# Kernel tuning notes

Hardware: AMD Instinct MI355X
Metric: run time of the kernel (lower is better)

Reference implementation:

```python
import jax, jax.numpy as jnp
import numpy as np

N = 50000   # nodes per graph stream
E = 800000  # edges per graph stream
G = 100     # graphs in batch
FIN, H = 74, 256


def setup_inputs() -> dict:
    key = jax.random.key(0)
    ks = jax.random.split(key, 16)
    d = {
        'xl': jax.random.normal(ks[0], (N, FIN), jnp.float32),
        'xr': jax.random.normal(ks[1], (N, FIN), jnp.float32),
        'src_l': jax.random.randint(ks[2], (E,), 0, N, jnp.int32),
        'dst_l': jax.random.randint(ks[3], (E,), 0, N, jnp.int32),
        'src_r': jax.random.randint(ks[4], (E,), 0, N, jnp.int32),
        'dst_r': jax.random.randint(ks[5], (E,), 0, N, jnp.int32),
        'gid_l': jnp.sort(jax.random.randint(ks[6], (N,), 0, G, jnp.int32)),
        'gid_r': jnp.sort(jax.random.randint(ks[7], (N,), 0, G, jnp.int32)),
        'W0': jax.random.normal(ks[8], (FIN, H), jnp.float32) / np.sqrt(FIN),
        'b0': jnp.zeros((H,), jnp.float32),
        'W1': jax.random.normal(ks[9], (H, H), jnp.float32) / np.sqrt(H),
        'b1': jnp.zeros((H,), jnp.float32),
        'W2': jax.random.normal(ks[10], (H, H), jnp.float32) / np.sqrt(H),
        'b2': jnp.zeros((H,), jnp.float32),
        'Wf1': jax.random.normal(ks[11], (2 * H, H), jnp.float32) / np.sqrt(2 * H),
        'bf1': jnp.zeros((H,), jnp.float32),
        'Wf2': jax.random.normal(ks[12], (H, 1), jnp.float32) / np.sqrt(H),
        'bf2': jnp.zeros((1,), jnp.float32),
    }
    return d


def _deg_isqrt(idx, n):
    deg = jax.ops.segment_sum(jnp.ones_like(idx, jnp.float32), idx, num_segments=n)
    return jax.lax.rsqrt(jnp.maximum(deg, 1.0))


def _graph_conv(x, src, dst, do_isq, di_isq, W, b):
    # DGL GraphConv, norm='both': h = relu(D_in^{-1/2} A D_out^{-1/2} X W + b)
    h = (x * do_isq[:, None]) @ W            # transform-first (in_feats >= out for layer0 path is fine mathematically)
    agg = jax.ops.segment_sum(h[src], dst, num_segments=x.shape[0])
    return jax.nn.relu(agg * di_isq[:, None] + b)


def reference(xl, xr, src_l, dst_l, src_r, dst_r, gid_l, gid_r,
              W0, b0, W1, b1, W2, b2, Wf1, bf1, Wf2, bf2):
    do_l, di_l = _deg_isqrt(src_l, N), _deg_isqrt(dst_l, N)
    do_r, di_r = _deg_isqrt(src_r, N), _deg_isqrt(dst_r, N)
    Ws, bs = (W0, W1, W2), (b0, b1, b2)
    hl, hr = xl, xr
    for W, b in zip(Ws, bs):  # shared weights across both graph streams
        hl = _graph_conv(hl, src_l, dst_l, do_l, di_l, W, b)
        hr = _graph_conv(hr, src_r, dst_r, do_r, di_r, W, b)
    pl = jax.ops.segment_sum(hl, gid_l, num_segments=G)  # dgl.sum_nodes
    pr = jax.ops.segment_sum(hr, gid_r, num_segments=G)
    z = jnp.concatenate([pl, pr], axis=-1)               # [G, 2H]
    return jax.nn.relu(z @ Wf1 + bf1) @ Wf2 + bf2        # [G, 1]
```

## Files before the change

kernel.cpp:

```cpp
#include <hip/hip_runtime.h>

#define N_NODES 50000
#define N_EDGES 800000
#define N_GRAPHS 100
#define FIN_DIM 74
#define K0 96
#define H_DIM 256
#define EG 3125
#define XS_BLKS 18750
#define WCONV_BLKS 608
#define AGG0_BLKS 3128
#define AGGH_BLKS 6256
#define GEMM_BLKS 782
#define POOL_BLKS 782
#define SCAN_BLOCKS 196

typedef float f32x4 __attribute__((ext_vector_type(4)));
typedef unsigned int u32x4 __attribute__((ext_vector_type(4)));
typedef unsigned short us8 __attribute__((ext_vector_type(8)));
typedef __bf16 bf16x8 __attribute__((ext_vector_type(8)));

__device__ __forceinline__ unsigned short f2bf(float x) {
    unsigned u = __builtin_bit_cast(unsigned, x);
    u += 0x7fff + ((u >> 16) & 1);
    return (unsigned short)(u >> 16);
}
__device__ __forceinline__ float bf2f(unsigned short h) {
    return __builtin_bit_cast(float, (unsigned)h << 16);
}
__device__ __forceinline__ void acc8(float* a, us8 v) {
    u32x4 w = __builtin_bit_cast(u32x4, v);
    #pragma unroll
    for (int i = 0; i < 4; ++i) {
        a[2 * i]     += __builtin_bit_cast(float, w[i] << 16);
        a[2 * i + 1] += __builtin_bit_cast(float, w[i] & 0xffff0000u);
    }
}


__device__ __forceinline__ void hist_body(int bid, const int* __restrict__ src,
                                          const int* __restrict__ dst,
                                          int* __restrict__ cs, int* __restrict__ fc,
                                          int* __restrict__ rk) {
    int e = bid * 256 + threadIdx.x;
    if (e < N_EDGES) {
        rk[e] = atomicAdd(&fc[dst[e]], 1);
        atomicAdd(&cs[src[e]], 1);
    }
}

__device__ __forceinline__ void scat_body(int bid, const int* __restrict__ src,
                                          const int* __restrict__ dst,
                                          const int* __restrict__ rp,
                                          const int* __restrict__ rk,
                                          int* __restrict__ col) {
    int e = bid * 256 + threadIdx.x;
    if (e < N_EDGES) {
        int d = dst[e];
        col[rp[d] + rk[e]] = src[e];
    }
}

__device__ __forceinline__ void xscale_body(int bid, const float* __restrict__ x,
                                            const float* __restrict__ dso,
                                            unsigned short* __restrict__ xp) {
    int id = bid * 256 + threadIdx.x;
    int n = id / 96, f = id - n * 96;
    float v = (f < FIN_DIM) ? x[(size_t)n * FIN_DIM + f] * dso[n] : 0.f;
    xp[(size_t)(f >> 4) * (N_NODES * 16) + (size_t)n * 16 + (f & 15)] = f2bf(v);
}

__device__ __forceinline__ void wconv_body(int bid, const float* __restrict__ W0,
                                           const float* __restrict__ W1,
                                           const float* __restrict__ W2,
                                           unsigned short* __restrict__ Wt) {
    int id = bid * 256 + threadIdx.x;
    if (id < 256 * 96) {
        int n = id / 96, k = id - n * 96;
        float v = (k < FIN_DIM) ? W0[(size_t)k * H_DIM + n] : 0.f;
        Wt[id] = f2bf(v);
    } else if (id < 256 * 96 + 65536) {
        int id2 = id - 256 * 96;
        int n = id2 >> 8, k = id2 & 255;
        Wt[id] = f2bf(W1[(size_t)k * H_DIM + n]);
    } else {
        int id3 = id - 256 * 96 - 65536;
        int n = id3 >> 8, k = id3 & 255;
        Wt[id] = f2bf(W2[(size_t)k * H_DIM + n]);
    }
}

template<int SW, int NACT, int NSL>
__device__ __forceinline__ void agg_body(int abid, int cg,
                                         const unsigned short* __restrict__ h,
                                         const int* __restrict__ rp,
                                         const int* __restrict__ col,
                                         unsigned short* __restrict__ A) {
    const int CPB = SW / 8;
    const int NPB = 256 / CPB;
    if (cg >= NSL) return;
    int slot = threadIdx.x & (CPB - 1);
    int n = (abid >> 3) * NPB + threadIdx.x / CPB;
    if (n >= N_NODES) return;
    unsigned short* dst = A + (size_t)cg * (N_NODES * SW) + (size_t)n * SW + slot * 8;
    if (cg >= NACT) { us8 z = {}; *(us8*)dst = z; return; }
    const unsigned short* hs = h + (size_t)cg * (N_NODES * SW) + slot * 8;
    int beg = rp[n], end = rp[n + 1];
    float a[8] = {};
    int j = beg;
    for (; j + 3 < end; j += 4) {
        int s0 = col[j], s1 = col[j + 1], s2 = col[j + 2], s3 = col[j + 3];
        us8 v0 = *(const us8*)(hs + (size_t)s0 * SW);
        us8 v1 = *(const us8*)(hs + (size_t)s1 * SW);
        us8 v2 = *(const us8*)(hs + (size_t)s2 * SW);
        us8 v3 = *(const us8*)(hs + (size_t)s3 * SW);
        acc8(a, v0); acc8(a, v1); acc8(a, v2); acc8(a, v3);
    }
    for (; j < end; ++j)
        acc8(a, *(const us8*)(hs + (size_t)col[j] * SW));
    us8 r;
    #pragma unroll
    for (int i = 0; i < 8; ++i) r[i] = f2bf(a[i]);
    *(us8*)dst = r;
}

__device__ __forceinline__ void pool_body(int nb, const unsigned short* __restrict__ h,
                                          const int* __restrict__ gid,
                                          float* __restrict__ pool) {
    int n0 = nb * 64;
    int f = threadIdx.x;
    const unsigned short* hf = h + (size_t)(f >> 5) * (N_NODES * 32) + (f & 31);
    int end = min(n0 + 64, N_NODES);
    float acc = 0.0f;
    int gcur = gid[n0];
    for (int i = n0; i < end; ++i) {
        int g = gid[i];
        if (g != gcur) {
            atomicAdd(&pool[(size_t)gcur * H_DIM + f], acc);
            acc = 0.0f;
            gcur = g;
        }
        acc += bf2f(hf[(size_t)i * 32]);
    }
    atomicAdd(&pool[(size_t)gcur * H_DIM + f], acc);
}

template<int K, int SW>
__device__ __forceinline__ void gemm_body(int id, const unsigned short* __restrict__ A,
                                          const unsigned short* __restrict__ Wt,
                                          const float* __restrict__ bias,
                                          const float* __restrict__ dsi,
                                          const float* __restrict__ scale,
                                          unsigned short* __restrict__ C,
                                          unsigned short* smem) {
    unsigned short (*Ah)[40] = (unsigned short(*)[40])smem;
    unsigned short (*Bh)[40] = (unsigned short(*)[40])(smem + 128 * 40);
    const int M = N_NODES;

    int tid = threadIdx.x;
    int lane = tid & 63, wid = tid >> 6;
    int wm = (wid >> 1) * 64, wn = (wid & 1) * 64;
    int bm = (id >> 1) * 128, bn = (id & 1) * 128;

    f32x4 acc[4][4] = {};
    int r0 = wm + (lane & 15);
    int c0 = wn + (lane & 15);
    int kA = (lane >> 4) * 8;

    for (int k0 = 0; k0 < K; k0 += 32) {
        #pragma unroll
        for (int i = 0; i < 2; ++i) {
            int q = tid + i * 256;
            int row = q >> 2, k8 = (q & 3) * 8;
            int gm = bm + row;
            int kk = k0 + k8;
            us8 v = {};
            if (gm < M)
                v = *(const us8*)(A + (size_t)(kk / SW) * ((size_t)N_NODES * SW)
                                    + (size_t)gm * SW + (kk % SW));
            *(us8*)&Ah[row][k8] = v;
        }
        {
            int colx = tid & 127, kg = tid >> 7;
            const unsigned short* wsrc = Wt + (size_t)(bn + colx) * K + k0 + kg * 16;
            us8 w0 = *(const us8*)(wsrc);
            us8 w1 = *(const us8*)(wsrc + 8);
            *(us8*)&Bh[colx][kg * 16] = w0;
            *(us8*)&Bh[colx][kg * 16 + 8] = w1;
        }
        __syncthreads();

        bf16x8 ah[4], bh[4];
        #pragma unroll
        for (int m = 0; m < 4; ++m)
            ah[m] = __builtin_bit_cast(bf16x8, *(const us8*)&Ah[r0 + m * 16][kA]);
        #pragma unroll
        for (int n = 0; n < 4; ++n)
            bh[n] = __builtin_bit_cast(bf16x8, *(const us8*)&Bh[c0 + n * 16][kA]);

        #pragma unroll
        for (int m = 0; m < 4; ++m)
            #pragma unroll
            for (int n = 0; n < 4; ++n)
                acc[m][n] = __builtin_amdgcn_mfma_f32_16x16x32_bf16(ah[m], bh[n], acc[m][n], 0, 0, 0);
        __syncthreads();
    }

    int rowq = (lane >> 4) * 4;
    #pragma unroll
    for (int n = 0; n < 4; ++n) {
        int gn = bn + wn + n * 16 + (lane & 15);
        float bv = bias[gn];
        unsigned short* cs = C + (size_t)(gn >> 5) * (N_NODES * 32) + (gn & 31);
        #pragma unroll
        for (int m = 0; m < 4; ++m) {
            #pragma unroll
            for (int j = 0; j < 4; ++j) {
                int gm = bm + wm + m * 16 + rowq + j;
                if (gm < M) {
                    float r = fmaxf(acc[m][n][j] * dsi[gm] + bv, 0.0f);
                    if (scale) r *= scale[gm];
                    cs[(size_t)gm * 32] = f2bf(r);
                }
            }
        }
    }
}


__device__ __forceinline__ int block_excl_scan(int v, int* wsums) {
    int lane = threadIdx.x & 63, w = threadIdx.x >> 6;
    int x = v;
    #pragma unroll
    for (int ofs = 1; ofs < 64; ofs <<= 1) {
        int y = __shfl_up(x, ofs, 64);
        if (lane >= ofs) x += y;
    }
    if (lane == 63) wsums[w] = x;
    __syncthreads();
    int wo = 0;
    #pragma unroll
    for (int k = 0; k < 4; ++k) if (k < w) wo += wsums[k];
    return wo + x - v;
}

__global__ void k_hist2(const float* __restrict__ W0, const float* __restrict__ W1,
                        const float* __restrict__ W2, unsigned short* __restrict__ Wt,
                        const int* __restrict__ srcL, const int* __restrict__ dstL,
                        int* __restrict__ csL, int* __restrict__ fcL, int* __restrict__ rkL,
                        const int* __restrict__ srcR, const int* __restrict__ dstR,
                        int* __restrict__ csR, int* __restrict__ fcR, int* __restrict__ rkR) {
    int bid = blockIdx.x;
    if (bid < WCONV_BLKS)           wconv_body(bid, W0, W1, W2, Wt);
    else if (bid < WCONV_BLKS + EG) hist_body(bid - WCONV_BLKS, srcL, dstL, csL, fcL, rkL);
    else                            hist_body(bid - WCONV_BLKS - EG, srcR, dstR, csR, fcR, rkR);
}

__global__ void deg_scan1_kernel(const int* __restrict__ csL, const int* __restrict__ fcL,
                                 float* __restrict__ dsoL, float* __restrict__ dsiL,
                                 int* __restrict__ rpL, int* __restrict__ bsL,
                                 const int* __restrict__ csR, const int* __restrict__ fcR,
                                 float* __restrict__ dsoR, float* __restrict__ dsiR,
                                 int* __restrict__ rpR, int* __restrict__ bsR) {
    const int* cs = blockIdx.y ? csR : csL;
    const int* fc = blockIdx.y ? fcR : fcL;
    float* dso = blockIdx.y ? dsoR : dsoL;
    float* dsi = blockIdx.y ? dsiR : dsiL;
    int* rp = blockIdx.y ? rpR : rpL;
    int* bs = blockIdx.y ? bsR : bsL;
    __shared__ int ws[4];
    int i = blockIdx.x * 256 + threadIdx.x;
    int v = 0;
    if (i < N_NODES) {
        dso[i] = rsqrtf(fmaxf((float)cs[i], 1.0f));
        v = fc[i];
        dsi[i] = rsqrtf(fmaxf((float)v, 1.0f));
    }
    int ex = block_excl_scan(v, ws);
    if (i < N_NODES) rp[i] = ex;
    if (threadIdx.x == 255) bs[blockIdx.x] = ex + v;
}

__global__ void scan2_kernel(int* __restrict__ bsL, int* __restrict__ bsR, int nb) {
    int* bs = blockIdx.y ? bsR : bsL;
    __shared__ int ws[4];
    int i = threadIdx.x;
    int v = (i < nb) ? bs[i] : 0;
    int ex = block_excl_scan(v, ws);
    __syncthreads();
    if (i < nb) bs[i] = ex;
}

__global__ void scan3_kernel(int* __restrict__ rpL, const int* __restrict__ bsL,
                             int* __restrict__ rpR, const int* __restrict__ bsR) {
    int* rp = blockIdx.y ? rpR : rpL;
    const int* bs = blockIdx.y ? bsR : bsL;
    int i = blockIdx.x * 256 + threadIdx.x;
    if (i < N_NODES) rp[i] += bs[blockIdx.x];
    if (i == 0) rp[N_NODES] = N_EDGES;
}

__global__ void fuse_ssxx(const int* __restrict__ srcL, const int* __restrict__ dstL,
                          const int* __restrict__ rpL, const int* __restrict__ rkL,
                          int* __restrict__ colL,
                          const int* __restrict__ srcR, const int* __restrict__ dstR,
                          const int* __restrict__ rpR, const int* __restrict__ rkR,
                          int* __restrict__ colR,
                          const float* __restrict__ xL, const float* __restrict__ dsoL,
                          unsigned short* __restrict__ xpL,
                          const float* __restrict__ xR, const float* __restrict__ dsoR,
                          unsigned short* __restrict__ xpR) {
    int bid = blockIdx.x;
    if (bid < EG)                         scat_body(bid, srcL, dstL, rpL, rkL, colL);
    else if (bid < 2 * EG)                scat_body(bid - EG, srcR, dstR, rpR, rkR, colR);
    else if (bid < 2 * EG + XS_BLKS)      xscale_body(bid - 2 * EG, xL, dsoL, xpL);
    else                                  xscale_body(bid - 2 * EG - XS_BLKS, xR, dsoR, xpR);
}

template<int SW, int NACT, int NSL, int NB>
__global__ void fuse_agg2(const unsigned short* __restrict__ hL, const int* __restrict__ rpL,
                          const int* __restrict__ colL, unsigned short* __restrict__ AL,
                          const unsigned short* __restrict__ hR, const int* __restrict__ rpR,
                          const int* __restrict__ colR, unsigned short* __restrict__ AR) {
    int bid = blockIdx.x;
    if (bid < NB) agg_body<SW, NACT, NSL>(bid, bid & 7, hL, rpL, colL, AL);
    else {
        int lb = bid - NB;
        agg_body<SW, NACT, NSL>(lb, lb & 7, hR, rpR, colR, AR);
    }
}

template<int K, int SW>
__global__ __launch_bounds__(256) void gemm_pair2(
        const unsigned short* __restrict__ AL, const float* __restrict__ dsiL,
        const float* __restrict__ scL, unsigned short* __restrict__ CL,
        const unsigned short* __restrict__ AR, const float* __restrict__ dsiR,
        const float* __restrict__ scR, unsigned short* __restrict__ CR,
        const unsigned short* __restrict__ Wt, const float* __restrict__ bias) {
    __shared__ unsigned short smem[2 * 128 * 40];
    int bid = blockIdx.x;
    if (bid < GEMM_BLKS) gemm_body<K, SW>(bid, AL, Wt, bias, dsiL, scL, CL, smem);
    else                 gemm_body<K, SW>(bid - GEMM_BLKS, AR, Wt, bias, dsiR, scR, CR, smem);
}

__global__ void pool2_kernel(const unsigned short* __restrict__ hL, const int* __restrict__ gidL,
                             float* __restrict__ poolL,
                             const unsigned short* __restrict__ hR, const int* __restrict__ gidR,
                             float* __restrict__ poolR) {
    int bid = blockIdx.x;
    if (bid < POOL_BLKS) pool_body(bid, hL, gidL, poolL);
    else                 pool_body(bid - POOL_BLKS, hR, gidR, poolR);
}

__global__ __launch_bounds__(256) void mlp_kernel(
        const float* __restrict__ pl, const float* __restrict__ pr,
        const float* __restrict__ Wf1, const float* __restrict__ bf1,
        const float* __restrict__ Wf2, const float* __restrict__ bf2,
        float* __restrict__ out) {
    __shared__ float z[512];
    __shared__ float red[256];
    int g = blockIdx.x, tid = threadIdx.x;
    z[tid] = pl[(size_t)g * H_DIM + tid];
    z[tid + 256] = pr[(size_t)g * H_DIM + tid];
    __syncthreads();
    float t = bf1[tid];
    #pragma unroll 8
    for (int k = 0; k < 512; ++k) t += z[k] * Wf1[(size_t)k * H_DIM + tid];
    t = fmaxf(t, 0.0f);
    red[tid] = t * Wf2[tid];
    __syncthreads();
    for (int ofs = 128; ofs > 0; ofs >>= 1) {
        if (tid < ofs) red[tid] += red[tid + ofs];
        __syncthreads();
    }
    if (tid == 0) out[g] = red[0] + bf2[0];
}


extern "C" void kernel_launch(void* const* d_in, const int* in_sizes, int n_in,
                              void* d_out, int out_size, void* d_ws, size_t ws_size,
                              hipStream_t stream) {
    const float* xl   = (const float*)d_in[0];
    const float* xr   = (const float*)d_in[1];
    const int* src_l  = (const int*)d_in[2];
    const int* dst_l  = (const int*)d_in[3];
    const int* src_r  = (const int*)d_in[4];
    const int* dst_r  = (const int*)d_in[5];
    const int* gid_l  = (const int*)d_in[6];
    const int* gid_r  = (const int*)d_in[7];
    const float* W0   = (const float*)d_in[8];
    const float* b0   = (const float*)d_in[9];
    const float* W1   = (const float*)d_in[10];
    const float* b1   = (const float*)d_in[11];
    const float* W2   = (const float*)d_in[12];
    const float* b2   = (const float*)d_in[13];
    const float* Wf1  = (const float*)d_in[14];
    const float* bf1  = (const float*)d_in[15];
    const float* Wf2  = (const float*)d_in[16];
    const float* bf2  = (const float*)d_in[17];
    float* out = (float*)d_out;
    (void)in_sizes; (void)n_in; (void)out_size; (void)ws_size;

    size_t off = 0;
    auto carve = [&](size_t bytes) {
        void* p = (char*)d_ws + off;
        off += (bytes + 255) & ~(size_t)255;
        return p;
    };
    const size_t NB4 = (size_t)N_NODES * 4;

    char* zstart = (char*)d_ws;
    int*   cs_l   = (int*)carve(NB4);
    int*   fc_l   = (int*)carve(NB4);
    int*   cs_r   = (int*)carve(NB4);
    int*   fc_r   = (int*)carve(NB4);
    float* pool_l = (float*)carve((size_t)N_GRAPHS * H_DIM * 4);
    float* pool_r = (float*)carve((size_t)N_GRAPHS * H_DIM * 4);
    size_t zbytes = off;

    float* dso_l = (float*)carve(NB4);
    float* dsi_l = (float*)carve(NB4);
    float* dso_r = (float*)carve(NB4);
    float* dsi_r = (float*)carve(NB4);
    int*   rp_l  = (int*)carve((size_t)(N_NODES + 1) * 4);
    int*   rp_r  = (int*)carve((size_t)(N_NODES + 1) * 4);
    int*   col_l = (int*)carve((size_t)N_EDGES * 4);
    int*   col_r = (int*)carve((size_t)N_EDGES * 4);
    int*   rk_l  = (int*)carve((size_t)N_EDGES * 4);
    int*   rk_r  = (int*)carve((size_t)N_EDGES * 4);
    int*   bs_l  = (int*)carve((size_t)SCAN_BLOCKS * 4);
    int*   bs_r  = (int*)carve((size_t)SCAN_BLOCKS * 4);

    unsigned short* Wt    = (unsigned short*)carve((size_t)(256 * 96 + 2 * 65536) * 2);
    unsigned short* Wt0   = Wt;
    unsigned short* Wt1   = Wt + 256 * 96;
    unsigned short* Wt2   = Wt + 256 * 96 + 65536;
    unsigned short* xp_l  = (unsigned short*)carve((size_t)N_NODES * 96 * 2);
    unsigned short* xp_r  = (unsigned short*)carve((size_t)N_NODES * 96 * 2);
    unsigned short* bufA_l = (unsigned short*)carve((size_t)N_NODES * H_DIM * 2);
    unsigned short* bufA_r = (unsigned short*)carve((size_t)N_NODES * H_DIM * 2);
    unsigned short* bufH_l = (unsigned short*)carve((size_t)N_NODES * H_DIM * 2);
    unsigned short* bufH_r = (unsigned short*)carve((size_t)N_NODES * H_DIM * 2);

    hipMemsetAsync(zstart, 0, zbytes, stream);

    k_hist2<<<WCONV_BLKS + 2 * EG, 256, 0, stream>>>(
        W0, W1, W2, Wt,
        src_l, dst_l, cs_l, fc_l, rk_l,
        src_r, dst_r, cs_r, fc_r, rk_r);

    deg_scan1_kernel<<<dim3(SCAN_BLOCKS, 2), 256, 0, stream>>>(
        cs_l, fc_l, dso_l, dsi_l, rp_l, bs_l,
        cs_r, fc_r, dso_r, dsi_r, rp_r, bs_r);
    scan2_kernel<<<dim3(1, 2), 256, 0, stream>>>(bs_l, bs_r, SCAN_BLOCKS);
    scan3_kernel<<<dim3(SCAN_BLOCKS, 2), 256, 0, stream>>>(rp_l, bs_l, rp_r, bs_r);

    fuse_ssxx<<<2 * EG + 2 * XS_BLKS, 256, 0, stream>>>(
        src_l, dst_l, rp_l, rk_l, col_l,
        src_r, dst_r, rp_r, rk_r, col_r,
        xl, dso_l, xp_l,
        xr, dso_r, xp_r);

    fuse_agg2<16, 5, 6, AGG0_BLKS><<<2 * AGG0_BLKS, 256, 0, stream>>>(
        xp_l, rp_l, col_l, bufA_l,
        xp_r, rp_r, col_r, bufA_r);
    gemm_pair2<K0, 16><<<2 * GEMM_BLKS, 256, 0, stream>>>(
        bufA_l, dsi_l, dso_l, bufH_l,
        bufA_r, dsi_r, dso_r, bufH_r,
        Wt0, b0);

    fuse_agg2<32, 8, 8, AGGH_BLKS><<<2 * AGGH_BLKS, 256, 0, stream>>>(
        bufH_l, rp_l, col_l, bufA_l,
        bufH_r, rp_r, col_r, bufA_r);
    gemm_pair2<H_DIM, 32><<<2 * GEMM_BLKS, 256, 0, stream>>>(
        bufA_l, dsi_l, dso_l, bufH_l,
        bufA_r, dsi_r, dso_r, bufH_r,
        Wt1, b1);

    fuse_agg2<32, 8, 8, AGGH_BLKS><<<2 * AGGH_BLKS, 256, 0, stream>>>(
        bufH_l, rp_l, col_l, bufA_l,
        bufH_r, rp_r, col_r, bufA_r);
    gemm_pair2<H_DIM, 32><<<2 * GEMM_BLKS, 256, 0, stream>>>(
        bufA_l, dsi_l, nullptr, bufH_l,
        bufA_r, dsi_r, nullptr, bufH_r,
        Wt2, b2);

    pool2_kernel<<<2 * POOL_BLKS, 256, 0, stream>>>(
        bufH_l, gid_l, pool_l,
        bufH_r, gid_r, pool_r);
    mlp_kernel<<<N_GRAPHS, 256, 0, stream>>>(pool_l, pool_r, Wf1, bf1, Wf2, bf2, out);
}
```

Baseline: 747.6 us.

## Split hidden-layer aggregation into two feature-slice halves and vectorize x scaling

The hidden-layer aggregation is split into two launches. Each launch processes four of the eight feature slices for the left stream and the other four for the right stream, interleaved by block id. The aim is a smaller working set of gathered feature columns per launch, which should raise cache hit rates on the random neighbour gathers. The input scaling kernel now handles two features per thread with vector loads and stores, halving its block count. The risk is an extra launch and a changed slice-to-block mapping (grp<<3 as the block base), which must still cover every node correctly.

```diff
diff --git a/kernel.cpp b/kernel.cpp
--- a/kernel.cpp
+++ b/kernel.cpp
@@ -7,7 +7,7 @@
 #define K0 96
 #define H_DIM 256
 #define EG 3125
-#define XS_BLKS 18750
+#define XS2_BLKS 9375
 #define WCONV_BLKS 608
 #define AGG0_BLKS 3128
 #define AGGH_BLKS 6256
@@ -16,7 +16,9 @@
 #define SCAN_BLOCKS 196
 
 typedef float f32x4 __attribute__((ext_vector_type(4)));
+typedef float f32x2 __attribute__((ext_vector_type(2)));
 typedef unsigned int u32x4 __attribute__((ext_vector_type(4)));
+typedef unsigned short us2 __attribute__((ext_vector_type(2)));
 typedef unsigned short us8 __attribute__((ext_vector_type(8)));
 typedef __bf16 bf16x8 __attribute__((ext_vector_type(8)));
 
@@ -65,9 +67,15 @@
                                             const float* __restrict__ dso,
                                             unsigned short* __restrict__ xp) {
     int id = bid * 256 + threadIdx.x;
-    int n = id / 96, f = id - n * 96;
-    float v = (f < FIN_DIM) ? x[(size_t)n * FIN_DIM + f] * dso[n] : 0.f;
-    xp[(size_t)(f >> 4) * (N_NODES * 16) + (size_t)n * 16 + (f & 15)] = f2bf(v);
+    int n = id / 48, f = (id - n * 48) * 2;
+    float v0 = 0.f, v1 = 0.f;
+    if (f < FIN_DIM) {
+        f32x2 t = *(const f32x2*)&x[(size_t)n * FIN_DIM + f];
+        float d = dso[n];
+        v0 = t[0] * d; v1 = t[1] * d;
+    }
+    us2 r = { f2bf(v0), f2bf(v1) };
+    *(us2*)&xp[(size_t)(f >> 4) * (N_NODES * 16) + (size_t)n * 16 + (f & 15)] = r;
 }
 
 __device__ __forceinline__ void wconv_body(int bid, const float* __restrict__ W0,
@@ -313,21 +321,31 @@
     int bid = blockIdx.x;
     if (bid < EG)                         scat_body(bid, srcL, dstL, rpL, rkL, colL);
     else if (bid < 2 * EG)                scat_body(bid - EG, srcR, dstR, rpR, rkR, colR);
-    else if (bid < 2 * EG + XS_BLKS)      xscale_body(bid - 2 * EG, xL, dsoL, xpL);
-    else                                  xscale_body(bid - 2 * EG - XS_BLKS, xR, dsoR, xpR);
-}
-
-template<int SW, int NACT, int NSL, int NB>
-__global__ void fuse_agg2(const unsigned short* __restrict__ hL, const int* __restrict__ rpL,
-                          const int* __restrict__ colL, unsigned short* __restrict__ AL,
-                          const unsigned short* __restrict__ hR, const int* __restrict__ rpR,
-                          const int* __restrict__ colR, unsigned short* __restrict__ AR) {
+    else if (bid < 2 * EG + XS2_BLKS)     xscale_body(bid - 2 * EG, xL, dsoL, xpL);
+    else                                  xscale_body(bid - 2 * EG - XS2_BLKS, xR, dsoR, xpR);
+}
+
+__global__ void fuse_agg2_l0(const unsigned short* __restrict__ hL, const int* __restrict__ rpL,
+                             const int* __restrict__ colL, unsigned short* __restrict__ AL,
+                             const unsigned short* __restrict__ hR, const int* __restrict__ rpR,
+                             const int* __restrict__ colR, unsigned short* __restrict__ AR) {
     int bid = blockIdx.x;
-    if (bid < NB) agg_body<SW, NACT, NSL>(bid, bid & 7, hL, rpL, colL, AL);
+    if (bid < AGG0_BLKS) agg_body<16, 5, 6>(bid, bid & 7, hL, rpL, colL, AL);
     else {
-        int lb = bid - NB;
-        agg_body<SW, NACT, NSL>(lb, lb & 7, hR, rpR, colR, AR);
-    }
+        int lb = bid - AGG0_BLKS;
+        agg_body<16, 5, 6>(lb, lb & 7, hR, rpR, colR, AR);
+    }
+}
+
+template<int SOFF_L, int SOFF_R>
+__global__ void fuse_agg2_half(const unsigned short* __restrict__ hL, const int* __restrict__ rpL,
+                               const int* __restrict__ colL, unsigned short* __restrict__ AL,
+                               const unsigned short* __restrict__ hR, const int* __restrict__ rpR,
+                               const int* __restrict__ colR, unsigned short* __restrict__ AR) {
+    int bid = blockIdx.x;
+    int lane = bid & 7, grp = bid >> 3;
+    if (lane < 4) agg_body<32, 8, 8>(grp << 3, SOFF_L + lane, hL, rpL, colL, AL);
+    else          agg_body<32, 8, 8>(grp << 3, SOFF_R + (lane - 4), hR, rpR, colR, AR);
 }
 
 template<int K, int SW>
@@ -455,13 +473,13 @@
     scan2_kernel<<<dim3(1, 2), 256, 0, stream>>>(bs_l, bs_r, SCAN_BLOCKS);
     scan3_kernel<<<dim3(SCAN_BLOCKS, 2), 256, 0, stream>>>(rp_l, bs_l, rp_r, bs_r);
 
-    fuse_ssxx<<<2 * EG + 2 * XS_BLKS, 256, 0, stream>>>(
+    fuse_ssxx<<<2 * EG + 2 * XS2_BLKS, 256, 0, stream>>>(
         src_l, dst_l, rp_l, rk_l, col_l,
         src_r, dst_r, rp_r, rk_r, col_r,
         xl, dso_l, xp_l,
         xr, dso_r, xp_r);
 
-    fuse_agg2<16, 5, 6, AGG0_BLKS><<<2 * AGG0_BLKS, 256, 0, stream>>>(
+    fuse_agg2_l0<<<2 * AGG0_BLKS, 256, 0, stream>>>(
         xp_l, rp_l, col_l, bufA_l,
         xp_r, rp_r, col_r, bufA_r);
     gemm_pair2<K0, 16><<<2 * GEMM_BLKS, 256, 0, stream>>>(
@@ -469,7 +487,10 @@
         bufA_r, dsi_r, dso_r, bufH_r,
         Wt0, b0);
 
-    fuse_agg2<32, 8, 8, AGGH_BLKS><<<2 * AGGH_BLKS, 256, 0, stream>>>(
+    fuse_agg2_half<0, 4><<<AGGH_BLKS, 256, 0, stream>>>(
+        bufH_l, rp_l, col_l, bufA_l,
+        bufH_r, rp_r, col_r, bufA_r);
+    fuse_agg2_half<4, 0><<<AGGH_BLKS, 256, 0, stream>>>(
         bufH_l, rp_l, col_l, bufA_l,
         bufH_r, rp_r, col_r, bufA_r);
     gemm_pair2<H_DIM, 32><<<2 * GEMM_BLKS, 256, 0, stream>>>(
@@ -477,7 +498,10 @@
         bufA_r, dsi_r, dso_r, bufH_r,
         Wt1, b1);
 
-    fuse_agg2<32, 8, 8, AGGH_BLKS><<<2 * AGGH_BLKS, 256, 0, stream>>>(
+    fuse_agg2_half<0, 4><<<AGGH_BLKS, 256, 0, stream>>>(
+        bufH_l, rp_l, col_l, bufA_l,
+        bufH_r, rp_r, col_r, bufA_r);
+    fuse_agg2_half<4, 0><<<AGGH_BLKS, 256, 0, stream>>>(
         bufH_l, rp_l, col_l, bufA_l,
         bufH_r, rp_r, col_r, bufA_r);
     gemm_pair2<H_DIM, 32><<<2 * GEMM_BLKS, 256, 0, stream>>>(
```

New measurement: 748.4 us. No clear change (+0.1%).
